# Performance work log

Measured on AMD Instinct MI355X. Metric: run time of the kernel, lower is better.

Reference implementation:

```python
import jax, jax.numpy as jnp
import numpy as np
from jax import lax

B, S, C, D, V = 256, 50, 40, 256, 20000
T_DIFF = 1000
BETA_START, BETA_END = 1e-4, 2e-2


def _lstm(x, Wih, Whh, bih, bhh):
    # x: [B,S,D]; single-layer LSTM, batch_first, eval mode (no dropout)
    Bb = x.shape[0]
    H = Whh.shape[1]
    def step(carry, xt):
        h, c = carry
        g = xt @ Wih.T + bih + h @ Whh.T + bhh  # [B,4H]
        i, f, gg, o = jnp.split(g, 4, axis=-1)
        i = jax.nn.sigmoid(i); f = jax.nn.sigmoid(f)
        gg = jnp.tanh(gg); o = jax.nn.sigmoid(o)
        c = f * c + i * gg
        h = o * jnp.tanh(c)
        return (h, c), h
    h0 = jnp.zeros((Bb, H), x.dtype)
    (_, _), hs = lax.scan(step, (h0, h0), x.transpose(1, 0, 2))
    return hs.transpose(1, 0, 2)  # [B,S,H]


def setup_inputs() -> dict:
    key = jax.random.key(0)
    ks = jax.random.split(key, 20)
    sc = 0.05
    inp = {
        'input_seqs': jax.random.randint(ks[0], (B, S, C), 0, V),
        'masks': jnp.zeros((B, S), jnp.int32),
        'lengths': jax.random.randint(ks[1], (B,), 1, S + 1),
        'seq_time_step': jax.random.uniform(ks[2], (B, S), jnp.float32),
        'code_masks': jnp.zeros((B, S, C), jnp.int32),
        'diffusion_time_t': jax.random.randint(ks[3], (B,), 0, T_DIFF),
        'normal_noise': jax.random.normal(ks[4], (B, S, D), jnp.float32),
        # learned parameters
        'emb': jax.random.normal(ks[5], (V + 1, D), jnp.float32) * sc,
        'Wih': jax.random.normal(ks[6], (4 * D, D), jnp.float32) * sc,
        'Whh': jax.random.normal(ks[7], (4 * D, D), jnp.float32) * sc,
        'bih': jnp.zeros((4 * D,), jnp.float32),
        'bhh': jnp.zeros((4 * D,), jnp.float32),
        'Whk': jax.random.normal(ks[8], (D, D), jnp.float32) * sc,
        'bhk': jnp.zeros((D,), jnp.float32),
        'W1': jax.random.normal(ks[9], (64, 2 * D), jnp.float32) * sc,
        'b1': jnp.zeros((64,), jnp.float32),
        'W2': jax.random.normal(ks[10], (2, 64), jnp.float32) * sc,
        'b2': jnp.zeros((2,), jnp.float32),
        'Wdiff': jax.random.normal(ks[11], (D, D), jnp.float32) * sc,
        'bdiff': jnp.zeros((D,), jnp.float32),
        'temb': jax.random.normal(ks[12], (T_DIFF, D), jnp.float32) * sc,
        'Wout': jax.random.normal(ks[13], (2, D), jnp.float32) * sc,
        'bout': jnp.zeros((2,), jnp.float32),
    }
    # padding_idx row zeroed like nn.Embedding(padding_idx=-1)
    inp['emb'] = inp['emb'].at[V].set(0.0)
    return inp


def reference(input_seqs, masks, lengths, seq_time_step, code_masks,
              diffusion_time_t, normal_noise,
              emb, Wih, Whh, bih, bhh, Whk, bhk, W1, b1, W2, b2,
              Wdiff, bdiff, temb, Wout, bout):
    # embedding sum over codes per visit
    x = emb[input_seqs].sum(axis=2)  # [B,S,D]
    rnn_out = _lstm(x, Wih, Whh, bih, bhh)  # [B,S,D]

    # vectorized alignment loop: e_k is ALWAYS x[:,0] (as in source),
    # position i>=1 attends between e_k and w_hk(rnn_out[i-1])
    w = rnn_out @ Whk.T + bhk  # [B,S,D]
    e_k = x[:, :1, :]  # [B,1,D]
    wprev = w[:, :-1, :]  # [B,S-1,D] -> timestep i uses w[i-1]
    cat = jnp.concatenate([jnp.broadcast_to(e_k, wprev.shape), wprev], -1)
    attn = jax.nn.softmax(jnp.tanh(cat @ W1.T + b1) @ W2.T + b2, axis=-1)  # [B,S-1,2]
    aligned_rest = e_k * attn[..., 0:1] + wprev * attn[..., 1:2]
    aligned_e_t = jnp.concatenate([e_k, aligned_rest], axis=1)  # [B,S,D]

    # diffusion noising (linear beta schedule as in ehr.yml defaults)
    betas = jnp.linspace(BETA_START, BETA_END, T_DIFF, dtype=jnp.float32)
    alpha = jnp.cumprod(1.0 - betas)[diffusion_time_t][:, None, None]
    noisy = aligned_e_t * jnp.sqrt(alpha) + normal_noise * jnp.sqrt(1.0 - alpha)

    # UNet surrogate (source unavailable): timestep-conditioned linear map
    predicted_noise = (noisy + temb[diffusion_time_t][:, None, :]) @ Wdiff + bdiff

    gen_x = aligned_e_t + (normal_noise - predicted_noise)
    pool_x = jnp.max(x, axis=1) @ Wout.T + bout  # [B,2]
    gen_pool_x = jnp.max(gen_x, axis=1) @ Wout.T + bout  # [B,2]
    return (pool_x, gen_pool_x, predicted_noise, normal_noise)
```

## Files before the change

kernel.cpp:

```cpp
#include <hip/hip_runtime.h>
#include <cmath>

#define Bb 256
#define Ss 50
#define Cc 40
#define Dd 256
#define Vv 20000

typedef __bf16 bf16;
typedef __bf16 bf16x8 __attribute__((ext_vector_type(8)));
typedef float f32x4 __attribute__((ext_vector_type(4)));
typedef unsigned long long u64;

#define GL2LDS(g, l) __builtin_amdgcn_global_load_lds( \
    (__attribute__((address_space(1))) void*)(g), \
    (__attribute__((address_space(3))) void*)(l), 16, 0, 0)

#define OFFB_GATES    0ull
#define OFFB_ALIGNED  0ull
#define OFFB_CAT      13107200ull
#define OFFB_TMPB     25952256ull
#define OFFB_H1       32505856ull
#define OFFB_ATTNW    35717120ull
#define OFFB_X        52428800ull
#define OFFB_XB       65536000ull
#define OFFB_RNNB     72089600ull
#define OFFB_W        78643200ull
#define OFFB_BAR      91750400ull
#define OFFB_WIHB     92012544ull
#define OFFB_WHHB     92536832ull
#define OFFB_WHKB     93061120ull
#define OFFB_W1B      93192192ull
#define OFFB_WDTB     93257728ull
#define OFFB_SALPHA   93388800ull
#define OFFB_SBETA    93389824ull

template<int BM, int BN, int ACT>
__global__ __launch_bounds__(256) void mfma_gemm(
    const bf16* __restrict__ A, int lda,
    const bf16* __restrict__ B, int ldb,
    const float* __restrict__ bias1, const float* __restrict__ bias2,
    float* __restrict__ C, int ldc, int K)
{
    constexpr int BK = 32;
    constexpr int NF = BN / 32;
    __shared__ bf16 As[BM * BK];
    __shared__ bf16 Bs[BN * BK];
    const int tid  = threadIdx.x;
    const int wave = tid >> 6;
    const int lane = tid & 63;
    const int m0 = blockIdx.x * BM;
    const int n0 = blockIdx.y * BN;
    const int wm = (wave >> 1) * 64;
    const int wn = (wave & 1) * (BN / 2);

    f32x4 acc[4][NF];
#pragma unroll
    for (int i = 0; i < 4; ++i)
#pragma unroll
        for (int j = 0; j < NF; ++j) acc[i][j] = (f32x4){0.f, 0.f, 0.f, 0.f};

    const int ar = tid >> 2;
    const int ac = tid & 3;
    const int sw = ac ^ (ar & 3);
    const int lr = lane & 15;
    const int q  = lane >> 4;

    for (int k0 = 0; k0 < K; k0 += BK) {
        __syncthreads();
#pragma unroll
        for (int it = 0; it < BM / 64; ++it) {
            const bf16* gp = A + (size_t)(m0 + it * 64 + ar) * lda + k0 + sw * 8;
            GL2LDS(gp, As + it * 2048 + wave * 512);
        }
#pragma unroll
        for (int it = 0; it < BN / 64; ++it) {
            const bf16* gp = B + (size_t)(n0 + it * 64 + ar) * ldb + k0 + sw * 8;
            GL2LDS(gp, Bs + it * 2048 + wave * 512);
        }
        __syncthreads();

        bf16x8 af[4], bfv[NF];
#pragma unroll
        for (int fm = 0; fm < 4; ++fm) {
            int m = wm + fm * 16 + lr;
            af[fm] = *(const bf16x8*)(As + m * 32 + ((q ^ (m & 3)) * 8));
        }
#pragma unroll
        for (int fn = 0; fn < NF; ++fn) {
            int n = wn + fn * 16 + lr;
            bfv[fn] = *(const bf16x8*)(Bs + n * 32 + ((q ^ (n & 3)) * 8));
        }
#pragma unroll
        for (int fm = 0; fm < 4; ++fm)
#pragma unroll
            for (int fn = 0; fn < NF; ++fn)
                acc[fm][fn] = __builtin_amdgcn_mfma_f32_16x16x32_bf16(
                    af[fm], bfv[fn], acc[fm][fn], 0, 0, 0);
    }

    const int rbase = q * 4;
#pragma unroll
    for (int fn = 0; fn < NF; ++fn) {
        const int col = n0 + wn + fn * 16 + lr;
        float bb = 0.f;
        if (bias1) bb += bias1[col];
        if (bias2) bb += bias2[col];
#pragma unroll
        for (int fm = 0; fm < 4; ++fm) {
            f32x4 v = acc[fm][fn];
#pragma unroll
            for (int r = 0; r < 4; ++r) {
                const int row = m0 + wm + fm * 16 + rbase + r;
                float val = v[r] + bb;
                if (ACT == 1) val = tanhf(val);
                C[(size_t)row * ldc + col] = val;
            }
        }
    }
}

__global__ __launch_bounds__(512, 2) void lstm_pair2(
    const bf16* __restrict__ Whhb,
    const float* __restrict__ gates,
    bf16* __restrict__ rnnb,
    unsigned* __restrict__ bar)
{
    __shared__ bf16 hbuf[2][16 * 256];
    const int tid  = threadIdx.x;
    const int w    = tid >> 6;
    const int lane = tid & 63;
    const int lr   = lane & 15;
    const int q    = lane >> 4;
    const int bm   = blockIdx.x & 15;
    const int bd   = blockIdx.x >> 4;
    const int pd   = 1 - bd;
    const int dg   = bd * 128 + w * 16 + lr;

    f32x4 wfr[4][8];
#pragma unroll
    for (int g = 0; g < 4; ++g) {
        const bf16* brow = Whhb + (size_t)(g * 256 + dg) * Dd + q * 8;
#pragma unroll
        for (int kc = 0; kc < 8; ++kc)
            wfr[g][kc] = *(const f32x4*)(brow + kc * 32);
    }
#pragma unroll
    for (int g = 0; g < 4; ++g)
        asm volatile("" : "+v"(wfr[g][0]), "+v"(wfr[g][1]), "+v"(wfr[g][2]),
                          "+v"(wfr[g][3]), "+v"(wfr[g][4]), "+v"(wfr[g][5]),
                          "+v"(wfr[g][6]), "+v"(wfr[g][7]));

    const float* gp[4];
#pragma unroll
    for (int r = 0; r < 4; ++r)
        gp[r] = gates + (size_t)(bm * 16 + q * 4 + r) * (Ss * 1024) + dg;

    const int xrow = tid >> 5;
    const int xc8  = tid & 31;
    const size_t my_base = ((size_t)(bm * 16 + xrow) * Ss) * Dd + bd * 128 + xc8 * 4;
    const size_t pt_base = ((size_t)(bm * 16 + xrow) * Ss) * Dd + pd * 128 + xc8 * 4;
    const int pack_off = xrow * 512 + (((bd * 16 + (xc8 >> 1)) ^ (xrow & 7)) << 4) + (xc8 & 1) * 8;
    const int unp_off  = xrow * 512 + (((pd * 16 + (xc8 >> 1)) ^ (xrow & 7)) << 4) + (xc8 & 1) * 8;
    unsigned* myf = bar + (bm * 2 + bd) * 32;
    unsigned* pf  = bar + (bm * 2 + pd) * 32;

    int ew_off[4];
#pragma unroll
    for (int r = 0; r < 4; ++r) {
        const int row = q * 4 + r;
        ew_off[r] = row * 512 + (((dg >> 3) ^ (row & 7)) << 4) + (dg & 7) * 2;
    }

    float c[4] = {0.f, 0.f, 0.f, 0.f};
    float gaA[4][4], gaB[4][4];
#pragma unroll
    for (int r = 0; r < 4; ++r)
#pragma unroll
        for (int g = 0; g < 4; ++g) gaA[g][r] = gp[r][g * 256];

#define LSTEP(T, GACUR, GANEXT, RD, WR, DOREAD, DOPF)                           \
    {                                                                           \
        if (DOPF) {                                                             \
            _Pragma("unroll")                                                   \
            for (int r = 0; r < 4; ++r)                                         \
                _Pragma("unroll")                                               \
                for (int g = 0; g < 4; ++g)                                     \
                    GANEXT[g][r] = gp[r][(size_t)((T) + 1) * 1024 + g * 256];   \
        }                                                                       \
        f32x4 acc[4];                                                           \
        _Pragma("unroll")                                                       \
        for (int g = 0; g < 4; ++g) acc[g] = (f32x4){0.f, 0.f, 0.f, 0.f};       \
        if (DOREAD) {                                                           \
            bf16x8 af[4];                                                       \
            _Pragma("unroll")                                                   \
            for (int kc = 0; kc < 4; ++kc)                                      \
                af[kc] = *(const bf16x8*)((const char*)(RD) + lr * 512          \
                         + (((kc * 4 + q) ^ (lr & 7)) << 4));                   \
            _Pragma("unroll")                                                   \
            for (int kc = 0; kc < 4; ++kc)                                      \
                _Pragma("unroll")                                               \
                for (int g = 0; g < 4; ++g)                                     \
                    acc[g] = __builtin_amdgcn_mfma_f32_16x16x32_bf16(           \
                        af[kc], __builtin_bit_cast(bf16x8, wfr[g][kc]),         \
                        acc[g], 0, 0, 0);                                       \
            _Pragma("unroll")                                                   \
            for (int kc = 0; kc < 4; ++kc)                                      \
                af[kc] = *(const bf16x8*)((const char*)(RD) + lr * 512          \
                         + ((((kc + 4) * 4 + q) ^ (lr & 7)) << 4));             \
            _Pragma("unroll")                                                   \
            for (int kc = 0; kc < 4; ++kc)                                      \
                _Pragma("unroll")                                               \
                for (int g = 0; g < 4; ++g)                                     \
                    acc[g] = __builtin_amdgcn_mfma_f32_16x16x32_bf16(           \
                        af[kc], __builtin_bit_cast(bf16x8, wfr[g][kc + 4]),     \
                        acc[g], 0, 0, 0);                                       \
        }                                                                       \
        _Pragma("unroll")                                                       \
        for (int r = 0; r < 4; ++r) {                                           \
            float gi = acc[0][r] + GACUR[0][r];                                 \
            float gf = acc[1][r] + GACUR[1][r];                                 \
            float gg = acc[2][r] + GACUR[2][r];                                 \
            float go = acc[3][r] + GACUR[3][r];                                 \
            float ii  = 1.f / (1.f + expf(-gi));                                \
            float ff  = 1.f / (1.f + expf(-gf));                                \
            float g2t = tanhf(gg);                                              \
            float oo  = 1.f / (1.f + expf(-go));                                \
            c[r] = ff * c[r] + ii * g2t;                                        \
            *(bf16*)((char*)(WR) + ew_off[r]) = (bf16)(oo * tanhf(c[r]));       \
        }                                                                       \
        __syncthreads();   \
        {                                                                       \
            u64 v = *(const u64*)((const char*)(WR) + pack_off);                \
            __hip_atomic_store((u64*)(rnnb + my_base + (size_t)(T) * Dd), v,    \
                               __ATOMIC_RELAXED, __HIP_MEMORY_SCOPE_AGENT);     \
        }                                                                       \
        if ((T) != Ss - 1) {                                                    \
            __syncthreads();        \
            if (tid == 0)                                                       \
                __hip_atomic_store(myf, (unsigned)((T) + 1),                    \
                                   __ATOMIC_RELAXED, __HIP_MEMORY_SCOPE_AGENT); \
            while (__hip_atomic_load(pf, __ATOMIC_RELAXED,                      \
                                     __HIP_MEMORY_SCOPE_AGENT)                  \
                   < (unsigned)((T) + 1)) {}                                    \
            u64 rv = __hip_atomic_load(                                         \
                (const u64*)(rnnb + pt_base + (size_t)(T) * Dd),                \
                __ATOMIC_RELAXED, __HIP_MEMORY_SCOPE_AGENT);                    \
            *(u64*)((char*)(WR) + unp_off) = rv;                                \
            __syncthreads();                \
        }                                                                       \
    }

    for (int t2 = 0; t2 < Ss; t2 += 2) {
        LSTEP(t2,     gaA, gaB, hbuf[1], hbuf[0], (t2 > 0), true);
        LSTEP(t2 + 1, gaB, gaA, hbuf[0], hbuf[1], true, (t2 + 2 < Ss));
    }
#undef LSTEP
}

__global__ __launch_bounds__(256) void cvt_bf16_kernel(
    const float* __restrict__ src, bf16* __restrict__ dst, int n)
{
    int i = blockIdx.x * 256 + threadIdx.x;
    if (i < n) dst[i] = (bf16)src[i];
}

__global__ __launch_bounds__(256) void transpose_cvt_kernel(
    const float* __restrict__ in, bf16* __restrict__ out, int R, int C)
{
    __shared__ float t[32][33];
    const int c0 = blockIdx.x * 32, r0 = blockIdx.y * 32;
    const int tx = threadIdx.x & 31, ty = threadIdx.x >> 5;
    for (int i = ty; i < 32; i += 8)
        t[i][tx] = in[(size_t)(r0 + i) * C + c0 + tx];
    __syncthreads();
    for (int i = ty; i < 32; i += 8)
        out[(size_t)(c0 + i) * R + r0 + tx] = (bf16)t[tx][i];
}

__global__ void alpha_kernel(const int* __restrict__ tdiff,
                             float* __restrict__ salpha, float* __restrict__ sbeta,
                             unsigned* __restrict__ bar)
{
    const int b = threadIdx.x;
#pragma unroll
    for (int j = 0; j < 4; ++j) bar[b * 4 + j] = 0u;
    const int t = tdiff[b];
    const float step = (0.02f - 1e-4f) / 999.f;
    float prod = 1.f;
    for (int j = 0; j <= t; ++j) prod *= (1.f - (1e-4f + j * step));
    salpha[b] = sqrtf(prod);
    sbeta[b]  = sqrtf(fmaxf(1.f - prod, 0.f));
}

__global__ __launch_bounds__(256) void embed_kernel(
    const int* __restrict__ seqs, const float* __restrict__ emb,
    float* __restrict__ x, bf16* __restrict__ xb)
{
    __shared__ int idx[Cc];
    const int bs = blockIdx.x;
    const int tid = threadIdx.x;
    if (tid < Cc) idx[tid] = seqs[(size_t)bs * Cc + tid];
    __syncthreads();
    float s = 0.f;
#pragma unroll 8
    for (int c = 0; c < Cc; ++c) s += emb[(size_t)idx[c] * Dd + tid];
    x[(size_t)bs * Dd + tid]  = s;
    xb[(size_t)bs * Dd + tid] = (bf16)s;
}

__global__ __launch_bounds__(256) void cat_build_kernel(
    const float* __restrict__ x, const float* __restrict__ w, bf16* __restrict__ cat)
{
    const int r = blockIdx.x;
    const int b = r / (Ss - 1), t = r % (Ss - 1);
    const int d = threadIdx.x;
    cat[(size_t)r * 512 + d]       = (bf16)x[((size_t)b * Ss) * Dd + d];
    cat[(size_t)r * 512 + 256 + d] = (bf16)w[((size_t)b * Ss + t) * Dd + d];
}

__global__ __launch_bounds__(256) void attn2_kernel(
    const float* __restrict__ H1, const float* __restrict__ W2,
    const float* __restrict__ b2, float* __restrict__ attnw)
{
    const int r = blockIdx.x * 4 + (threadIdx.x >> 6);
    const int j = threadIdx.x & 63;
    float h = H1[(size_t)r * 64 + j];
    float v0 = h * W2[j];
    float v1 = h * W2[64 + j];
#pragma unroll
    for (int off = 32; off; off >>= 1) { v0 += __shfl_down(v0, off); v1 += __shfl_down(v1, off); }
    if (j == 0) {
        float z0 = v0 + b2[0], z1 = v1 + b2[1];
        float m = fmaxf(z0, z1);
        float e0 = expf(z0 - m), e1 = expf(z1 - m);
        float inv = 1.f / (e0 + e1);
        attnw[(size_t)r * 2 + 0] = e0 * inv;
        attnw[(size_t)r * 2 + 1] = e1 * inv;
    }
}

__global__ __launch_bounds__(256) void attn_apply_kernel(
    const float* __restrict__ x, const float* __restrict__ w,
    const float* __restrict__ attnw, float* __restrict__ aligned)
{
    const int bs = blockIdx.x;
    const int b = bs / Ss, s = bs % Ss;
    const int d = threadIdx.x;
    const float ek = x[((size_t)b * Ss) * Dd + d];
    float v;
    if (s == 0) {
        v = ek;
    } else {
        const int r = b * (Ss - 1) + (s - 1);
        const float a0 = attnw[(size_t)r * 2], a1 = attnw[(size_t)r * 2 + 1];
        v = ek * a0 + w[((size_t)b * Ss + s - 1) * Dd + d] * a1;
    }
    aligned[(size_t)bs * Dd + d] = v;
}

__global__ __launch_bounds__(256) void diff_kernel(
    const float* __restrict__ aligned, const float* __restrict__ noise,
    const float* __restrict__ temb, const int* __restrict__ tdiff,
    const float* __restrict__ salpha, const float* __restrict__ sbeta,
    bf16* __restrict__ tmpb)
{
    const int bs = blockIdx.x;
    const int b = bs / Ss;
    const int d = threadIdx.x;
    const size_t i = (size_t)bs * Dd + d;
    const int t = tdiff[b];
    tmpb[i] = (bf16)(aligned[i] * salpha[b] + noise[i] * sbeta[b] + temb[(size_t)t * Dd + d]);
}

__device__ inline void pool_reduce_write(float m, const float* __restrict__ Wout,
                                         const float* __restrict__ bout,
                                         float* __restrict__ outp, int b,
                                         float* r0, float* r1)
{
    float v0 = m * Wout[threadIdx.x];
    float v1 = m * Wout[Dd + threadIdx.x];
#pragma unroll
    for (int off = 32; off; off >>= 1) { v0 += __shfl_down(v0, off); v1 += __shfl_down(v1, off); }
    const int lane = threadIdx.x & 63, wv = threadIdx.x >> 6;
    if (lane == 0) { r0[wv] = v0; r1[wv] = v1; }
    __syncthreads();
    if (threadIdx.x == 0) {
        outp[b * 2 + 0] = r0[0] + r0[1] + r0[2] + r0[3] + bout[0];
        outp[b * 2 + 1] = r1[0] + r1[1] + r1[2] + r1[3] + bout[1];
    }
}

__global__ __launch_bounds__(256) void pool_x_kernel(
    const float* __restrict__ x, const float* __restrict__ Wout,
    const float* __restrict__ bout, float* __restrict__ outp)
{
    __shared__ float r0[4], r1[4];
    const int b = blockIdx.x, d = threadIdx.x;
    float m = -INFINITY;
    for (int s = 0; s < Ss; ++s) m = fmaxf(m, x[((size_t)b * Ss + s) * Dd + d]);
    pool_reduce_write(m, Wout, bout, outp, b, r0, r1);
}

__global__ __launch_bounds__(256) void gen_pool_kernel(
    const float* __restrict__ aligned, const float* __restrict__ noise,
    const float* __restrict__ pred, const float* __restrict__ Wout,
    const float* __restrict__ bout, float* __restrict__ outp)
{
    __shared__ float r0[4], r1[4];
    const int b = blockIdx.x, d = threadIdx.x;
    float m = -INFINITY;
    for (int s = 0; s < Ss; ++s) {
        const size_t i = ((size_t)b * Ss + s) * Dd + d;
        m = fmaxf(m, aligned[i] + noise[i] - pred[i]);
    }
    pool_reduce_write(m, Wout, bout, outp, b, r0, r1);
}

extern "C" void kernel_launch(void* const* d_in, const int* in_sizes, int n_in,
                              void* d_out, int out_size, void* d_ws, size_t ws_size,
                              hipStream_t stream)
{
    const int*   seqs  = (const int*)d_in[0];
    const int*   tdiff = (const int*)d_in[5];
    const float* noise = (const float*)d_in[6];
    const float* emb   = (const float*)d_in[7];
    const float* Wih   = (const float*)d_in[8];
    const float* Whh   = (const float*)d_in[9];
    const float* bih   = (const float*)d_in[10];
    const float* bhh   = (const float*)d_in[11];
    const float* Whk   = (const float*)d_in[12];
    const float* bhk   = (const float*)d_in[13];
    const float* W1    = (const float*)d_in[14];
    const float* b1    = (const float*)d_in[15];
    const float* W2    = (const float*)d_in[16];
    const float* b2    = (const float*)d_in[17];
    const float* Wdiff = (const float*)d_in[18];
    const float* bdiff = (const float*)d_in[19];
    const float* temb  = (const float*)d_in[20];
    const float* Wout  = (const float*)d_in[21];
    const float* bout  = (const float*)d_in[22];

    float* outp = (float*)d_out;
    char*  wsb  = (char*)d_ws;

    float* gates   = (float*)(wsb + OFFB_GATES);
    float* aligned = (float*)(wsb + OFFB_ALIGNED);
    bf16*  catb    = (bf16*) (wsb + OFFB_CAT);
    bf16*  tmpb    = (bf16*) (wsb + OFFB_TMPB);
    float* H1      = (float*)(wsb + OFFB_H1);
    float* attnw   = (float*)(wsb + OFFB_ATTNW);
    float* x       = (float*)(wsb + OFFB_X);
    bf16*  xb      = (bf16*) (wsb + OFFB_XB);
    bf16*  rnnb    = (bf16*) (wsb + OFFB_RNNB);
    float* wbuf    = (float*)(wsb + OFFB_W);
    unsigned* bar  = (unsigned*)(wsb + OFFB_BAR);
    bf16*  Wihb    = (bf16*) (wsb + OFFB_WIHB);
    bf16*  Whhb    = (bf16*) (wsb + OFFB_WHHB);
    bf16*  Whkb    = (bf16*) (wsb + OFFB_WHKB);
    bf16*  W1b     = (bf16*) (wsb + OFFB_W1B);
    bf16*  WdTb    = (bf16*) (wsb + OFFB_WDTB);
    float* salpha  = (float*)(wsb + OFFB_SALPHA);
    float* sbeta   = (float*)(wsb + OFFB_SBETA);

    float* pred_out  = outp + 1024;
    float* noise_out = outp + 1024 + (size_t)Bb * Ss * Dd;

    alpha_kernel<<<1, 256, 0, stream>>>(tdiff, salpha, sbeta, bar);

    cvt_bf16_kernel<<<1024, 256, 0, stream>>>(Wih, Wihb, 262144);
    cvt_bf16_kernel<<<1024, 256, 0, stream>>>(Whh, Whhb, 262144);
    cvt_bf16_kernel<<<256,  256, 0, stream>>>(Whk, Whkb, 65536);
    cvt_bf16_kernel<<<128,  256, 0, stream>>>(W1,  W1b,  32768);
    transpose_cvt_kernel<<<dim3(8, 8), 256, 0, stream>>>(Wdiff, WdTb, 256, 256);

    embed_kernel<<<Bb * Ss, 256, 0, stream>>>(seqs, emb, x, xb);

    pool_x_kernel<<<Bb, 256, 0, stream>>>(x, Wout, bout, outp);

    mfma_gemm<128, 128, 0><<<dim3(100, 8), 256, 0, stream>>>(
        xb, 256, Wihb, 256, bih, bhh, gates, 1024, 256);

    lstm_pair2<<<32, 512, 0, stream>>>(Whhb, gates, rnnb, bar);

    mfma_gemm<128, 128, 0><<<dim3(100, 2), 256, 0, stream>>>(
        rnnb, 256, Whkb, 256, bhk, nullptr, wbuf, 256, 256);

    cat_build_kernel<<<Bb * (Ss - 1), 256, 0, stream>>>(x, wbuf, catb);
    mfma_gemm<128, 64, 1><<<dim3(98, 1), 256, 0, stream>>>(
        catb, 512, W1b, 512, b1, nullptr, H1, 64, 512);
    attn2_kernel<<<(Bb * (Ss - 1)) / 4, 256, 0, stream>>>(H1, W2, b2, attnw);
    attn_apply_kernel<<<Bb * Ss, 256, 0, stream>>>(x, wbuf, attnw, aligned);

    diff_kernel<<<Bb * Ss, 256, 0, stream>>>(aligned, noise, temb, tdiff, salpha, sbeta, tmpb);

    mfma_gemm<128, 128, 0><<<dim3(100, 2), 256, 0, stream>>>(
        tmpb, 256, WdTb, 256, bdiff, nullptr, pred_out, 256, 256);

    gen_pool_kernel<<<Bb, 256, 0, stream>>>(aligned, noise, pred_out, Wout, bout, outp + 512);

    hipMemcpyAsync(noise_out, noise, (size_t)Bb * Ss * Dd * sizeof(float),
                   hipMemcpyDeviceToDevice, stream);
}
```

Measured before the change: 504.4 us.

## Merge weight-prep launches, fuse attention apply with diffusion noising, pin LSTM weights in AGPRs

Folds the five weight conversion/transpose kernels and the alpha/barrier-reset kernel into one prep launch that dispatches by block index. Fuses attn_apply and diff into one kernel, so the aligned tensor no longer has to be re-read from memory. Changes the LSTM register pin constraint from VGPRs to AGPRs and re-applies the pin every step pair, to free VGPR pressure in the recurrent loop. Keeping the weights in AGPRs may add accvgpr read moves before each MFMA.

```diff
diff --git a/kernel.cpp b/kernel.cpp
--- a/kernel.cpp
+++ b/kernel.cpp
@@ -145,11 +145,13 @@
         for (int kc = 0; kc < 8; ++kc)
             wfr[g][kc] = *(const f32x4*)(brow + kc * 32);
     }
-#pragma unroll
-    for (int g = 0; g < 4; ++g)
-        asm volatile("" : "+v"(wfr[g][0]), "+v"(wfr[g][1]), "+v"(wfr[g][2]),
-                          "+v"(wfr[g][3]), "+v"(wfr[g][4]), "+v"(wfr[g][5]),
-                          "+v"(wfr[g][6]), "+v"(wfr[g][7]));
+#define PIN_W()                                                                \
+    _Pragma("unroll")                                                          \
+    for (int g = 0; g < 4; ++g)                                                \
+        asm volatile("" : "+a"(wfr[g][0]), "+a"(wfr[g][1]), "+a"(wfr[g][2]),   \
+                          "+a"(wfr[g][3]), "+a"(wfr[g][4]), "+a"(wfr[g][5]),   \
+                          "+a"(wfr[g][6]), "+a"(wfr[g][7]))
+    PIN_W();
 
     const float* gp[4];
 #pragma unroll
@@ -252,45 +254,52 @@
     }
 
     for (int t2 = 0; t2 < Ss; t2 += 2) {
+        PIN_W();
         LSTEP(t2,     gaA, gaB, hbuf[1], hbuf[0], (t2 > 0), true);
         LSTEP(t2 + 1, gaB, gaA, hbuf[0], hbuf[1], true, (t2 + 2 < Ss));
     }
 #undef LSTEP
-}
-
-__global__ __launch_bounds__(256) void cvt_bf16_kernel(
-    const float* __restrict__ src, bf16* __restrict__ dst, int n)
-{
-    int i = blockIdx.x * 256 + threadIdx.x;
-    if (i < n) dst[i] = (bf16)src[i];
-}
-
-__global__ __launch_bounds__(256) void transpose_cvt_kernel(
-    const float* __restrict__ in, bf16* __restrict__ out, int R, int C)
+#undef PIN_W
+}
+
+__global__ __launch_bounds__(256) void prep_kernel(
+    const float* __restrict__ Wih, bf16* __restrict__ Wihb,
+    const float* __restrict__ Whh, bf16* __restrict__ Whhb,
+    const float* __restrict__ Whk, bf16* __restrict__ Whkb,
+    const float* __restrict__ W1,  bf16* __restrict__ W1b,
+    const float* __restrict__ Wdiff, bf16* __restrict__ WdTb,
+    const int* __restrict__ tdiff, float* __restrict__ salpha,
+    float* __restrict__ sbeta, unsigned* __restrict__ bar)
 {
     __shared__ float t[32][33];
-    const int c0 = blockIdx.x * 32, r0 = blockIdx.y * 32;
-    const int tx = threadIdx.x & 31, ty = threadIdx.x >> 5;
-    for (int i = ty; i < 32; i += 8)
-        t[i][tx] = in[(size_t)(r0 + i) * C + c0 + tx];
-    __syncthreads();
-    for (int i = ty; i < 32; i += 8)
-        out[(size_t)(c0 + i) * R + r0 + tx] = (bf16)t[tx][i];
-}
-
-__global__ void alpha_kernel(const int* __restrict__ tdiff,
-                             float* __restrict__ salpha, float* __restrict__ sbeta,
-                             unsigned* __restrict__ bar)
-{
-    const int b = threadIdx.x;
-#pragma unroll
-    for (int j = 0; j < 4; ++j) bar[b * 4 + j] = 0u;
-    const int t = tdiff[b];
+    int bx = blockIdx.x;
+    const int tid = threadIdx.x;
+    if (bx < 1024) { int i = bx * 256 + tid; Wihb[i] = (bf16)Wih[i]; return; }
+    bx -= 1024;
+    if (bx < 1024) { int i = bx * 256 + tid; Whhb[i] = (bf16)Whh[i]; return; }
+    bx -= 1024;
+    if (bx < 256)  { int i = bx * 256 + tid; Whkb[i] = (bf16)Whk[i]; return; }
+    bx -= 256;
+    if (bx < 128)  { int i = bx * 256 + tid; W1b[i]  = (bf16)W1[i];  return; }
+    bx -= 128;
+    if (bx < 64) {
+        const int c0 = (bx & 7) * 32, r0 = (bx >> 3) * 32;
+        const int tx = tid & 31, ty = tid >> 5;
+        for (int i = ty; i < 32; i += 8)
+            t[i][tx] = Wdiff[(size_t)(r0 + i) * 256 + c0 + tx];
+        __syncthreads();
+        for (int i = ty; i < 32; i += 8)
+            WdTb[(size_t)(c0 + i) * 256 + r0 + tx] = (bf16)t[tx][i];
+        return;
+    }
+#pragma unroll
+    for (int j = 0; j < 4; ++j) bar[tid * 4 + j] = 0u;
+    const int tt = tdiff[tid];
     const float step = (0.02f - 1e-4f) / 999.f;
     float prod = 1.f;
-    for (int j = 0; j <= t; ++j) prod *= (1.f - (1e-4f + j * step));
-    salpha[b] = sqrtf(prod);
-    sbeta[b]  = sqrtf(fmaxf(1.f - prod, 0.f));
+    for (int j = 0; j <= tt; ++j) prod *= (1.f - (1e-4f + j * step));
+    salpha[tid] = sqrtf(prod);
+    sbeta[tid]  = sqrtf(fmaxf(1.f - prod, 0.f));
 }
 
 __global__ __launch_bounds__(256) void embed_kernel(
@@ -340,9 +349,12 @@
     }
 }
 
-__global__ __launch_bounds__(256) void attn_apply_kernel(
+__global__ __launch_bounds__(256) void attn_diff_kernel(
     const float* __restrict__ x, const float* __restrict__ w,
-    const float* __restrict__ attnw, float* __restrict__ aligned)
+    const float* __restrict__ attnw, const float* __restrict__ noise,
+    const float* __restrict__ temb, const int* __restrict__ tdiff,
+    const float* __restrict__ salpha, const float* __restrict__ sbeta,
+    float* __restrict__ aligned, bf16* __restrict__ tmpb)
 {
     const int bs = blockIdx.x;
     const int b = bs / Ss, s = bs % Ss;
@@ -356,21 +368,10 @@
         const float a0 = attnw[(size_t)r * 2], a1 = attnw[(size_t)r * 2 + 1];
         v = ek * a0 + w[((size_t)b * Ss + s - 1) * Dd + d] * a1;
     }
-    aligned[(size_t)bs * Dd + d] = v;
-}
-
-__global__ __launch_bounds__(256) void diff_kernel(
-    const float* __restrict__ aligned, const float* __restrict__ noise,
-    const float* __restrict__ temb, const int* __restrict__ tdiff,
-    const float* __restrict__ salpha, const float* __restrict__ sbeta,
-    bf16* __restrict__ tmpb)
-{
-    const int bs = blockIdx.x;
-    const int b = bs / Ss;
-    const int d = threadIdx.x;
     const size_t i = (size_t)bs * Dd + d;
+    aligned[i] = v;
     const int t = tdiff[b];
-    tmpb[i] = (bf16)(aligned[i] * salpha[b] + noise[i] * sbeta[b] + temb[(size_t)t * Dd + d]);
+    tmpb[i] = (bf16)(v * salpha[b] + noise[i] * sbeta[b] + temb[(size_t)t * Dd + d]);
 }
 
 __device__ inline void pool_reduce_write(float m, const float* __restrict__ Wout,
@@ -466,13 +467,9 @@
     float* pred_out  = outp + 1024;
     float* noise_out = outp + 1024 + (size_t)Bb * Ss * Dd;
 
-    alpha_kernel<<<1, 256, 0, stream>>>(tdiff, salpha, sbeta, bar);
-
-    cvt_bf16_kernel<<<1024, 256, 0, stream>>>(Wih, Wihb, 262144);
-    cvt_bf16_kernel<<<1024, 256, 0, stream>>>(Whh, Whhb, 262144);
-    cvt_bf16_kernel<<<256,  256, 0, stream>>>(Whk, Whkb, 65536);
-    cvt_bf16_kernel<<<128,  256, 0, stream>>>(W1,  W1b,  32768);
-    transpose_cvt_kernel<<<dim3(8, 8), 256, 0, stream>>>(Wdiff, WdTb, 256, 256);
+    prep_kernel<<<2497, 256, 0, stream>>>(Wih, Wihb, Whh, Whhb, Whk, Whkb,
+                                          W1, W1b, Wdiff, WdTb,
+                                          tdiff, salpha, sbeta, bar);
 
     embed_kernel<<<Bb * Ss, 256, 0, stream>>>(seqs, emb, x, xb);
 
@@ -490,9 +487,9 @@
     mfma_gemm<128, 64, 1><<<dim3(98, 1), 256, 0, stream>>>(
         catb, 512, W1b, 512, b1, nullptr, H1, 64, 512);
     attn2_kernel<<<(Bb * (Ss - 1)) / 4, 256, 0, stream>>>(H1, W2, b2, attnw);
-    attn_apply_kernel<<<Bb * Ss, 256, 0, stream>>>(x, wbuf, attnw, aligned);
-
-    diff_kernel<<<Bb * Ss, 256, 0, stream>>>(aligned, noise, temb, tdiff, salpha, sbeta, tmpb);
+
+    attn_diff_kernel<<<Bb * Ss, 256, 0, stream>>>(
+        x, wbuf, attnw, noise, temb, tdiff, salpha, sbeta, aligned, tmpb);
 
     mfma_gemm<128, 128, 0><<<dim3(100, 2), 256, 0, stream>>>(
         tmpb, 256, WdTb, 256, bdiff, nullptr, pred_out, 256, 256);
```

Result: slower. 553.0 us (+9.6%).
